# Performance work log

Hardware: AMD Instinct MI355X
Metric: run time of the kernel (lower is better)

Reference implementation:

```python
import jax, jax.numpy as jnp
import numpy as np


def _laplacian_kernel(x, z, bandwidth):
    x_sq = jnp.sum(x * x, axis=-1, keepdims=True)          # [N, 1]
    z_sq = jnp.sum(z * z, axis=-1)[None, :]                # [1, M]
    d2 = x_sq + z_sq - 2.0 * jnp.einsum('nd,md->nm', x, z)  # [N, M]
    d = jnp.sqrt(jnp.maximum(d2, 0.0))
    return jnp.exp(-d / bandwidth)


def setup_inputs() -> dict:
    key = jax.random.key(0)
    k1, k2, k3 = jax.random.split(key, 3)
    N, M, D, Y = 8192, 20000, 1024, 256
    batch = jax.random.normal(k1, (N, D), dtype=jnp.float32)
    centers = jax.random.normal(k2, (M, D), dtype=jnp.float32)
    weight = jax.random.normal(k3, (M, Y), dtype=jnp.float32) * 0.02
    return {"batch": batch, "centers": centers, "weight": weight, "bandwidth": 10}


def reference(batch, centers, weight, bandwidth):
    kmat = _laplacian_kernel(batch, centers, float(bandwidth))  # [N, M]
    pred = kmat @ weight                                        # [N, Y]
    return pred
```

## Files before the change

### kernel.cpp

```cpp
#include <hip/hip_runtime.h>
#include <stdint.h>

#define N_ROWS 8192
#define D_DIM  1024
#define M_CENT 20000
#define M_PAD  20224
#define M_TILES 79
#define Y_DIM  256
#define BM 128
#define BN 256
#define BK 64
#define NCHUNK 16
#define MSPLIT 4
#define TILES_PER_SPLIT 20
#define LDSP_STRIDE 264

#define BUFE 24576
#define ZOFF 8192
#define POFF 24576
#define LDS_ALL_E 58368

typedef __attribute__((ext_vector_type(4))) float  f32x4;
typedef __attribute__((ext_vector_type(8))) __bf16 bf16x8;

__device__ __forceinline__ unsigned short f2bf(float f) {
    union { float f; unsigned u; } v; v.f = f;
    unsigned u = v.u;
    u += 0x7FFFu + ((u >> 16) & 1u);
    return (unsigned short)(u >> 16);
}

__device__ __forceinline__ void gll16(void* lds, const void* g) {
    __builtin_amdgcn_global_load_lds(
        (const __attribute__((address_space(1))) void*)g,
        (__attribute__((address_space(3))) void*)lds, 16, 0, 0);
}

__global__ void cast_rows_kernel(const float* __restrict__ src,
                                 unsigned short* __restrict__ dst,
                                 float* __restrict__ sq, int nrows_valid) {
    int row = blockIdx.x;
    int t = threadIdx.x;
    float s = 0.f;
    if (row < nrows_valid) {
        float4 v = ((const float4*)(src + (size_t)row * D_DIM))[t];
        s = v.x * v.x + v.y * v.y + v.z * v.z + v.w * v.w;
        ushort4 o;
        o.x = f2bf(v.x); o.y = f2bf(v.y); o.z = f2bf(v.z); o.w = f2bf(v.w);
        ((ushort4*)(dst + (size_t)row * D_DIM))[t] = o;
    } else {
        ((ushort4*)(dst + (size_t)row * D_DIM))[t] = make_ushort4(0, 0, 0, 0);
    }
    __shared__ float red[4];
    for (int off = 32; off; off >>= 1) s += __shfl_down(s, off, 64);
    if ((t & 63) == 0) red[t >> 6] = s;
    __syncthreads();
    if (t == 0) sq[row] = red[0] + red[1] + red[2] + red[3];
}

__global__ void cast_wT_kernel(const float* __restrict__ w,
                               unsigned short* __restrict__ wT) {
    __shared__ float tile[32][33];
    int k0 = blockIdx.x * 32;
    int y0 = blockIdx.y * 32;
    int tx = threadIdx.x & 31;
    int ty = threadIdx.x >> 5;
    #pragma unroll
    for (int i = 0; i < 4; ++i) {
        int k = k0 + ty + i * 8;
        float v = (k < M_CENT) ? w[(size_t)k * Y_DIM + y0 + tx] : 0.f;
        tile[tx][ty + i * 8] = v;
    }
    __syncthreads();
    #pragma unroll
    for (int i = 0; i < 4; ++i) {
        int yl = ty + i * 8;
        wT[(size_t)(y0 + yl) * M_PAD + k0 + tx] = f2bf(tile[yl][tx]);
    }
}


#define STAGE(PAR, M0, KBASE) do {                                            \
    _Pragma("unroll")                                                         \
    for (int i_ = 0; i_ < 2; ++i_) {                  \
        int lin_ = t + i_ * 512;                                              \
        int row_ = lin_ >> 3, c_ = lin_ & 7;                                  \
        gll16(&lds_all[(PAR) * BUFE + lin_ * 8],                              \
              Xb + (size_t)(row0 + row_) * D_DIM + (KBASE) +                  \
                  ((c_ ^ (row_ & 7)) * 8));                                   \
    }                                                                         \
    _Pragma("unroll")                                                         \
    for (int i_ = 0; i_ < 4; ++i_) {                  \
        int lin_ = t + i_ * 512;                                              \
        int row_ = lin_ >> 3, c_ = lin_ & 7;                                  \
        gll16(&lds_all[(PAR) * BUFE + ZOFF + lin_ * 8],                       \
              Zb + (size_t)((M0) + row_) * D_DIM + (KBASE) +                  \
                  ((c_ ^ (row_ & 7)) * 8));                                   \
    } } while (0)

#define CHUNK(PAR, M0N, KBN) do {                                             \
    asm volatile("" ::: "memory");                                            \
    __builtin_amdgcn_s_barrier();                  \
    asm volatile("" ::: "memory");                                            \
    STAGE(PAR ^ 1, M0N, KBN);                                                 \
    __builtin_amdgcn_sched_barrier(0);                                        \
    asm volatile("s_waitcnt vmcnt(6)" ::: "memory");   \
    __builtin_amdgcn_s_barrier();            \
    asm volatile("" ::: "memory");                                            \
    _Pragma("unroll")                                                         \
    for (int kt_ = 0; kt_ < 2; ++kt_) {                                       \
        const int sw_ = ((kt_ * 4 + quad) ^ cx) * 8;                          \
        bf16x8 a_[4], b_[4];                                                  \
        _Pragma("unroll")                                                     \
        for (int it_ = 0; it_ < 4; ++it_)                                     \
            a_[it_] = *(const bf16x8*)&lds_all[(PAR) * BUFE +                 \
                (wx * 64 + it_ * 16 + l16) * BK + sw_];                       \
        _Pragma("unroll")                                                     \
        for (int jt_ = 0; jt_ < 4; ++jt_)                                     \
            b_[jt_] = *(const bf16x8*)&lds_all[(PAR) * BUFE + ZOFF +          \
                (wm * 64 + jt_ * 16 + l16) * BK + sw_];                       \
        __builtin_amdgcn_s_setprio(1);                                        \
        _Pragma("unroll")                                                     \
        for (int it_ = 0; it_ < 4; ++it_)                                     \
            _Pragma("unroll")                                                 \
            for (int jt_ = 0; jt_ < 4; ++jt_)                                 \
                S[it_ * 4 + jt_] = __builtin_amdgcn_mfma_f32_16x16x32_bf16(   \
                    a_[it_], b_[jt_], S[it_ * 4 + jt_], 0, 0, 0);             \
        __builtin_amdgcn_s_setprio(0);                                        \
    } } while (0)

__global__ void __launch_bounds__(512, 2)
fused_kernel(const unsigned short* __restrict__ Xb,
             const unsigned short* __restrict__ Zb,
             const unsigned short* __restrict__ WbT,
             const float* __restrict__ xsq,
             const float* __restrict__ zsq,
             const int* __restrict__ bwp,
             float* __restrict__ out) {
    __shared__ unsigned short lds_all[LDS_ALL_E];
    __shared__ float lds_xsq[BM];

    const int t    = threadIdx.x;
    const int wave = t >> 6;
    const int wx   = wave >> 2;
    const int wm   = wave & 3;
    const int lane = t & 63;
    const int quad = lane >> 4;
    const int l16  = lane & 15;
    const int cx   = l16 & 7;

    const int row0 = blockIdx.x * BM;
    const int mt0  = blockIdx.y * TILES_PER_SPLIT;
    int mt_end = mt0 + TILES_PER_SPLIT;
    if (mt_end > M_TILES) mt_end = M_TILES;

    int bwi = *bwp;
    float bw;
    if (bwi > 0 && bwi < 1000000) bw = (float)bwi;
    else { union { int i; float f; } u; u.i = bwi; bw = u.f; }
    const float inv_bw = 1.0f / bw;

    if (t < BM) lds_xsq[t] = xsq[row0 + t];

    const f32x4 vzero = {0.f, 0.f, 0.f, 0.f};
    f32x4 Oacc[16];
    #pragma unroll
    for (int i = 0; i < 16; ++i) Oacc[i] = vzero;

    STAGE(0, mt0 * BN, 0);
    __builtin_amdgcn_sched_barrier(0);

    for (int mt = mt0; mt < mt_end; ++mt) {
        const int m0 = mt * BN;
        const int m0next = (mt + 1 < mt_end) ? m0 + BN : m0;

        float zq[4];
        #pragma unroll
        for (int jt = 0; jt < 4; ++jt)
            zq[jt] = zsq[m0 + wm * 64 + jt * 16 + l16];

        f32x4 S[16];
        #pragma unroll
        for (int i = 0; i < 16; ++i) S[i] = vzero;

        #pragma unroll 1
        for (int kc = 0; kc < NCHUNK; kc += 2) {
            const bool last = (kc + 2 == NCHUNK);
            CHUNK(0, m0, (kc + 1) * BK);
            CHUNK(1, last ? m0next : m0, last ? 0 : (kc + 2) * BK);
        }

        asm volatile("" ::: "memory");
        __builtin_amdgcn_s_barrier();
        asm volatile("" ::: "memory");

        #pragma unroll
        for (int it = 0; it < 4; ++it) {
            #pragma unroll
            for (int jt = 0; jt < 4; ++jt) {
                f32x4 s4 = S[it * 4 + jt];
                const int col = wm * 64 + jt * 16 + l16;
                #pragma unroll
                for (int r = 0; r < 4; ++r) {
                    const int row = wx * 64 + it * 16 + quad * 4 + r;
                    float d2 = lds_xsq[row] + zq[jt] - 2.0f * s4[r];
                    d2 = fmaxf(d2, 0.f);
                    float p = __expf(-sqrtf(d2) * inv_bw);
                    lds_all[POFF + row * LDSP_STRIDE + col] = f2bf(p);
                }
            }
        }
        asm volatile("s_waitcnt lgkmcnt(0)" ::: "memory");
        __builtin_amdgcn_s_barrier();
        asm volatile("" ::: "memory");

        #pragma unroll
        for (int ks = 0; ks < 8; ++ks) {
            const int koff = ks * 32 + quad * 8;
            bf16x8 a[4], b[4];
            #pragma unroll
            for (int rt = 0; rt < 4; ++rt)
                a[rt] = *(const bf16x8*)&lds_all[POFF +
                    (wx * 64 + rt * 16 + l16) * LDSP_STRIDE + koff];
            #pragma unroll
            for (int ct = 0; ct < 4; ++ct) {
                const int y = wm * 64 + ct * 16 + l16;
                b[ct] = *(const bf16x8*)(WbT + (size_t)y * M_PAD + m0 + koff);
            }
            __builtin_amdgcn_s_setprio(1);
            #pragma unroll
            for (int rt = 0; rt < 4; ++rt)
                #pragma unroll
                for (int ct = 0; ct < 4; ++ct)
                    Oacc[rt * 4 + ct] = __builtin_amdgcn_mfma_f32_16x16x32_bf16(
                        a[rt], b[ct], Oacc[rt * 4 + ct], 0, 0, 0);
            __builtin_amdgcn_s_setprio(0);
        }
    }

    asm volatile("s_waitcnt vmcnt(0)" ::: "memory");

    #pragma unroll
    for (int rt = 0; rt < 4; ++rt) {
        #pragma unroll
        for (int ct = 0; ct < 4; ++ct) {
            f32x4 v = Oacc[rt * 4 + ct];
            const int y = wm * 64 + ct * 16 + l16;
            #pragma unroll
            for (int r = 0; r < 4; ++r) {
                const int row = row0 + wx * 64 + rt * 16 + quad * 4 + r;
                atomicAdd(&out[(size_t)row * Y_DIM + y], v[r]);
            }
        }
    }
}

extern "C" void kernel_launch(void* const* d_in, const int* in_sizes, int n_in,
                              void* d_out, int out_size, void* d_ws, size_t ws_size,
                              hipStream_t stream) {
    const float* X = (const float*)d_in[0];
    const float* Z = (const float*)d_in[1];
    const float* W = (const float*)d_in[2];
    const int*  bw = (const int*)d_in[3];
    float* out = (float*)d_out;

    char* ws = (char*)d_ws;
    size_t off = 0;
    unsigned short* Xb  = (unsigned short*)(ws + off); off += (size_t)N_ROWS * D_DIM * 2;
    unsigned short* Zb  = (unsigned short*)(ws + off); off += (size_t)M_PAD * D_DIM * 2;
    unsigned short* WbT = (unsigned short*)(ws + off); off += (size_t)Y_DIM * M_PAD * 2;
    float* xsq = (float*)(ws + off); off += (size_t)N_ROWS * 4;
    float* zsq = (float*)(ws + off); off += (size_t)M_PAD * 4;

    hipMemsetAsync(d_out, 0, (size_t)out_size * sizeof(float), stream);
    cast_rows_kernel<<<N_ROWS, 256, 0, stream>>>(X, Xb, xsq, N_ROWS);
    cast_rows_kernel<<<M_PAD, 256, 0, stream>>>(Z, Zb, zsq, M_CENT);
    cast_wT_kernel<<<dim3(M_PAD / 32, Y_DIM / 32), 256, 0, stream>>>(W, WbT);
    fused_kernel<<<dim3(N_ROWS / BM, MSPLIT), 512, 0, stream>>>(
        Xb, Zb, WbT, xsq, zsq, bw, out);
}
```

Baseline: 816.7 us.

## Shrink row tile to 64 with 4-wave blocks and double the M-split

The fused kernel moves from 128-row, 8-wave blocks to 64-row, 4-wave blocks. Each wave now covers all 64 rows and its own 64 centers, and the M dimension is split 8 ways instead of 4, giving four times as many blocks. Row norms are held in registers instead of LDS, and sqrt becomes a raw v_sqrt_f32 instruction. The trade-off is more blocks and more parallelism against less reuse of each staged Z tile across rows, more Z and W traffic per output, and twice as many atomic adds into the output.

```diff
diff --git a/kernel.cpp b/kernel.cpp
--- a/kernel.cpp
+++ b/kernel.cpp
@@ -7,18 +7,17 @@
 #define M_PAD  20224
 #define M_TILES 79
 #define Y_DIM  256
-#define BM 128
+#define BM 64
 #define BN 256
 #define BK 64
 #define NCHUNK 16
-#define MSPLIT 4
-#define TILES_PER_SPLIT 20
+#define MSPLIT 8
+#define TILES_PER_SPLIT 10
 #define LDSP_STRIDE 264
 
-#define BUFE 24576
-#define ZOFF 8192
-#define POFF 24576
-#define LDS_ALL_E 58368
+#define BUFE 20480
+#define ZOFF 4096
+#define POFF 20480
 
 typedef __attribute__((ext_vector_type(4))) float  f32x4;
 typedef __attribute__((ext_vector_type(8))) __bf16 bf16x8;
@@ -82,16 +81,16 @@
 
 #define STAGE(PAR, M0, KBASE) do {                                            \
     _Pragma("unroll")                                                         \
-    for (int i_ = 0; i_ < 2; ++i_) {                  \
-        int lin_ = t + i_ * 512;                                              \
+    for (int i_ = 0; i_ < 2; ++i_) {                   \
+        int lin_ = t + i_ * 256;                                              \
         int row_ = lin_ >> 3, c_ = lin_ & 7;                                  \
         gll16(&lds_all[(PAR) * BUFE + lin_ * 8],                              \
               Xb + (size_t)(row0 + row_) * D_DIM + (KBASE) +                  \
                   ((c_ ^ (row_ & 7)) * 8));                                   \
     }                                                                         \
     _Pragma("unroll")                                                         \
-    for (int i_ = 0; i_ < 4; ++i_) {                  \
-        int lin_ = t + i_ * 512;                                              \
+    for (int i_ = 0; i_ < 8; ++i_) {                  \
+        int lin_ = t + i_ * 256;                                              \
         int row_ = lin_ >> 3, c_ = lin_ & 7;                                  \
         gll16(&lds_all[(PAR) * BUFE + ZOFF + lin_ * 8],                       \
               Zb + (size_t)((M0) + row_) * D_DIM + (KBASE) +                  \
@@ -104,7 +103,7 @@
     asm volatile("" ::: "memory");                                            \
     STAGE(PAR ^ 1, M0N, KBN);                                                 \
     __builtin_amdgcn_sched_barrier(0);                                        \
-    asm volatile("s_waitcnt vmcnt(6)" ::: "memory");   \
+    asm volatile("s_waitcnt vmcnt(10)" ::: "memory");     \
     __builtin_amdgcn_s_barrier();            \
     asm volatile("" ::: "memory");                                            \
     _Pragma("unroll")                                                         \
@@ -114,11 +113,11 @@
         _Pragma("unroll")                                                     \
         for (int it_ = 0; it_ < 4; ++it_)                                     \
             a_[it_] = *(const bf16x8*)&lds_all[(PAR) * BUFE +                 \
-                (wx * 64 + it_ * 16 + l16) * BK + sw_];                       \
+                (it_ * 16 + l16) * BK + sw_];                                 \
         _Pragma("unroll")                                                     \
         for (int jt_ = 0; jt_ < 4; ++jt_)                                     \
             b_[jt_] = *(const bf16x8*)&lds_all[(PAR) * BUFE + ZOFF +          \
-                (wm * 64 + jt_ * 16 + l16) * BK + sw_];                       \
+                (wave * 64 + jt_ * 16 + l16) * BK + sw_];                     \
         __builtin_amdgcn_s_setprio(1);                                        \
         _Pragma("unroll")                                                     \
         for (int it_ = 0; it_ < 4; ++it_)                                     \
@@ -129,7 +128,7 @@
         __builtin_amdgcn_s_setprio(0);                                        \
     } } while (0)
 
-__global__ void __launch_bounds__(512, 2)
+__global__ void __launch_bounds__(256, 2)
 fused_kernel(const unsigned short* __restrict__ Xb,
              const unsigned short* __restrict__ Zb,
              const unsigned short* __restrict__ WbT,
@@ -137,13 +136,10 @@
              const float* __restrict__ zsq,
              const int* __restrict__ bwp,
              float* __restrict__ out) {
-    __shared__ unsigned short lds_all[LDS_ALL_E];
-    __shared__ float lds_xsq[BM];
+    __shared__ unsigned short lds_all[2 * BUFE];
 
     const int t    = threadIdx.x;
     const int wave = t >> 6;
-    const int wx   = wave >> 2;
-    const int wm   = wave & 3;
     const int lane = t & 63;
     const int quad = lane >> 4;
     const int l16  = lane & 15;
@@ -160,7 +156,10 @@
     else { union { int i; float f; } u; u.i = bwi; bw = u.f; }
     const float inv_bw = 1.0f / bw;
 
-    if (t < BM) lds_xsq[t] = xsq[row0 + t];
+    f32x4 xq[4];
+    #pragma unroll
+    for (int it = 0; it < 4; ++it)
+        xq[it] = *(const f32x4*)(xsq + row0 + it * 16 + quad * 4);
 
     const f32x4 vzero = {0.f, 0.f, 0.f, 0.f};
     f32x4 Oacc[16];
@@ -177,7 +176,7 @@
         float zq[4];
         #pragma unroll
         for (int jt = 0; jt < 4; ++jt)
-            zq[jt] = zsq[m0 + wm * 64 + jt * 16 + l16];
+            zq[jt] = zsq[m0 + wave * 64 + jt * 16 + l16];
 
         f32x4 S[16];
         #pragma unroll
@@ -199,13 +198,15 @@
             #pragma unroll
             for (int jt = 0; jt < 4; ++jt) {
                 f32x4 s4 = S[it * 4 + jt];
-                const int col = wm * 64 + jt * 16 + l16;
+                const int col = wave * 64 + jt * 16 + l16;
                 #pragma unroll
                 for (int r = 0; r < 4; ++r) {
-                    const int row = wx * 64 + it * 16 + quad * 4 + r;
-                    float d2 = lds_xsq[row] + zq[jt] - 2.0f * s4[r];
+                    const int row = it * 16 + quad * 4 + r;
+                    float d2 = xq[it][r] + zq[jt] - 2.0f * s4[r];
                     d2 = fmaxf(d2, 0.f);
-                    float p = __expf(-sqrtf(d2) * inv_bw);
+                    float d;
+                    asm("v_sqrt_f32 %0, %1" : "=v"(d) : "v"(d2));
+                    float p = __expf(-d * inv_bw);
                     lds_all[POFF + row * LDSP_STRIDE + col] = f2bf(p);
                 }
             }
@@ -221,10 +222,10 @@
             #pragma unroll
             for (int rt = 0; rt < 4; ++rt)
                 a[rt] = *(const bf16x8*)&lds_all[POFF +
-                    (wx * 64 + rt * 16 + l16) * LDSP_STRIDE + koff];
+                    (rt * 16 + l16) * LDSP_STRIDE + koff];
             #pragma unroll
             for (int ct = 0; ct < 4; ++ct) {
-                const int y = wm * 64 + ct * 16 + l16;
+                const int y = wave * 64 + ct * 16 + l16;
                 b[ct] = *(const bf16x8*)(WbT + (size_t)y * M_PAD + m0 + koff);
             }
             __builtin_amdgcn_s_setprio(1);
@@ -245,10 +246,10 @@
         #pragma unroll
         for (int ct = 0; ct < 4; ++ct) {
             f32x4 v = Oacc[rt * 4 + ct];
-            const int y = wm * 64 + ct * 16 + l16;
+            const int y = wave * 64 + ct * 16 + l16;
             #pragma unroll
             for (int r = 0; r < 4; ++r) {
-                const int row = row0 + wx * 64 + rt * 16 + quad * 4 + r;
+                const int row = row0 + rt * 16 + quad * 4 + r;
                 atomicAdd(&out[(size_t)row * Y_DIM + y], v[r]);
             }
         }
@@ -276,6 +277,6 @@
     cast_rows_kernel<<<N_ROWS, 256, 0, stream>>>(X, Xb, xsq, N_ROWS);
     cast_rows_kernel<<<M_PAD, 256, 0, stream>>>(Z, Zb, zsq, M_CENT);
     cast_wT_kernel<<<dim3(M_PAD / 32, Y_DIM / 32), 256, 0, stream>>>(W, WbT);
-    fused_kernel<<<dim3(N_ROWS / BM, MSPLIT), 512, 0, stream>>>(
+    fused_kernel<<<dim3(N_ROWS / BM, MSPLIT), 256, 0, stream>>>(
         Xb, Zb, WbT, xsq, zsq, bw, out);
 }
```

Result: faster. 778.0 us (-4.7%).
